# Kernel tuning notes

Hardware: AMD Instinct MI355X
Metric: run time of the kernel (lower is better)

Reference implementation:

```python
import jax, jax.numpy as jnp
import numpy as np

NUM_USERS = 200000
NUM_ITEMS = 100000
DIM = 64
NUM_LAYERS = 2
NUM_EDGES = 3200000
EPS = 1e-12  # F.normalize eps


def setup_inputs() -> dict:
    key = jax.random.key(0)
    ks = jax.random.split(key, 8)
    return {
        "user_emb": jax.random.normal(ks[0], (NUM_USERS, DIM), dtype=jnp.float32),
        "item_emb": jax.random.normal(ks[1], (NUM_ITEMS, DIM), dtype=jnp.float32),
        "Wu": jax.random.normal(ks[2], (NUM_LAYERS, DIM, 2 * DIM), dtype=jnp.float32) * 0.1,
        "Wi": jax.random.normal(ks[3], (NUM_LAYERS, DIM, 2 * DIM), dtype=jnp.float32) * 0.1,
        "u_idx": jax.random.randint(ks[4], (NUM_EDGES,), 0, NUM_USERS, dtype=jnp.int32),
        "i_idx": jax.random.randint(ks[5], (NUM_EDGES,), 0, NUM_ITEMS, dtype=jnp.int32),
        "w_u2i": jax.random.uniform(ks[6], (NUM_EDGES,), dtype=jnp.float32),
        "w_i2u": jax.random.uniform(ks[7], (NUM_EDGES,), dtype=jnp.float32),
    }


def _l2_normalize(x):
    # matches F.normalize(p=2, dim=1): x / max(||x||, eps)
    n = jnp.sqrt(jnp.sum(x * x, axis=1, keepdims=True))
    return x / jnp.maximum(n, EPS)


def _spmm(vals, rows, cols, h, num_rows):
    # (sparse [num_rows, num_cols]) @ h : gather rows of h at cols, scale, scatter-add
    msg = vals[:, None] * h[cols]  # [E, DIM]
    return jax.ops.segment_sum(msg, rows, num_segments=num_rows)


def reference(user_emb, item_emb, Wu, Wi, u_idx, i_idx, w_u2i, w_i2u):
    h_u, h_i = user_emb, item_emb
    for l in range(NUM_LAYERS):
        neigh_u = _spmm(w_u2i, u_idx, i_idx, h_i, NUM_USERS)   # adj_u2i @ h_i
        neigh_i = _spmm(w_i2u, i_idx, u_idx, h_u, NUM_ITEMS)   # adj_i2u @ h_u
        # Linear(2*dim -> dim, no bias): concat then x @ W.T
        h_u_new = jax.nn.relu(jnp.concatenate([h_u, neigh_u], axis=1) @ Wu[l].T)
        h_i_new = jax.nn.relu(jnp.concatenate([h_i, neigh_i], axis=1) @ Wi[l].T)
        h_u = _l2_normalize(h_u_new)
        h_i = _l2_normalize(h_i_new)
    return (h_u, h_i)
```

## Files before the change

kernel.cpp:

```cpp
#include <hip/hip_runtime.h>


#define N_USERS 200000
#define N_ITEMS 100000
#define N_EDGES 3200000
#define NB_U 782
#define NB_I 391

typedef float v2f __attribute__((ext_vector_type(2)));

__global__ __launch_bounds__(256) void wprep_kernel(
    const float* __restrict__ Wu, const float* __restrict__ Wi,
    float* __restrict__ WuT, float* __restrict__ WiT)
{
    int idx = blockIdx.x * 256 + threadIdx.x;
    const float* src = Wu;
    float* dst = WuT;
    int i = idx;
    if (idx >= 16384) { src = Wi; dst = WiT; i = idx - 16384; }
    int l = i >> 13;
    int r = i & 8191;
    int j = r >> 7;
    int k = r & 127;
    dst[l * 8192 + k * 64 + j] = src[i];
}

__global__ __launch_bounds__(256) void hist_kernel(
    const int* __restrict__ u_idx, const int* __restrict__ i_idx,
    int* __restrict__ deg_u, int* __restrict__ deg_i,
    unsigned short* __restrict__ rank_u, unsigned short* __restrict__ rank_i)
{
    int t = blockIdx.x * 256 + threadIdx.x;
    if (t < N_EDGES) {
        rank_u[t] = (unsigned short)atomicAdd(&deg_u[u_idx[t]], 1);
    } else {
        int e = t - N_EDGES;
        rank_i[e] = (unsigned short)atomicAdd(&deg_i[i_idx[e]], 1);
    }
}

__global__ __launch_bounds__(256) void scanA_kernel(
    const int* __restrict__ deg_u, const int* __restrict__ deg_i,
    int* __restrict__ bsum_u, int* __restrict__ bsum_i)
{
    int b = blockIdx.x;
    const int* deg; int n; int* bs; int bb;
    if (b < NB_U) { deg = deg_u; n = N_USERS; bs = bsum_u; bb = b; }
    else          { deg = deg_i; n = N_ITEMS; bs = bsum_i; bb = b - NB_U; }
    int i = bb * 256 + threadIdx.x;
    int v = (i < n) ? deg[i] : 0;
    #pragma unroll
    for (int off = 1; off < 64; off <<= 1) v += __shfl_xor(v, off);
    __shared__ int ws4[4];
    int wv = threadIdx.x >> 6;
    if ((threadIdx.x & 63) == 0) ws4[wv] = v;
    __syncthreads();
    if (threadIdx.x == 0) bs[bb] = ws4[0] + ws4[1] + ws4[2] + ws4[3];
}

__global__ __launch_bounds__(1024) void scanB_kernel(
    const int* __restrict__ bsum_u, int* __restrict__ bpre_u,
    const int* __restrict__ bsum_i, int* __restrict__ bpre_i)
{
    __shared__ int s[1024];
    const int* src; int* dst; int n;
    if (blockIdx.x == 0) { src = bsum_u; dst = bpre_u; n = NB_U; }
    else                 { src = bsum_i; dst = bpre_i; n = NB_I; }
    int t = threadIdx.x;
    int v = (t < n) ? src[t] : 0;
    s[t] = v; __syncthreads();
    #pragma unroll
    for (int off = 1; off < 1024; off <<= 1) {
        int x = (t >= off) ? s[t - off] : 0;
        __syncthreads();
        s[t] += x;
        __syncthreads();
    }
    if (t < n) dst[t] = s[t] - v;
}

__global__ __launch_bounds__(256) void scanC_kernel(
    const int* __restrict__ deg_u, const int* __restrict__ deg_i,
    const int* __restrict__ bpre_u, const int* __restrict__ bpre_i,
    int* __restrict__ rowptr_u, int* __restrict__ rowptr_i)
{
    int b = blockIdx.x;
    const int* deg; int n; const int* bpre; int* rowptr; int bb;
    if (b < NB_U) { deg = deg_u; n = N_USERS; bpre = bpre_u; rowptr = rowptr_u; bb = b; }
    else          { deg = deg_i; n = N_ITEMS; bpre = bpre_i; rowptr = rowptr_i; bb = b - NB_U; }
    int t = threadIdx.x;
    int i = bb * 256 + t;
    int d = (i < n) ? deg[i] : 0;
    __shared__ int s[256];
    s[t] = d; __syncthreads();
    #pragma unroll
    for (int off = 1; off < 256; off <<= 1) {
        int x = (t >= off) ? s[t - off] : 0;
        __syncthreads();
        s[t] += x;
        __syncthreads();
    }
    int val = bpre[bb] + (s[t] - d);
    if (i < n) rowptr[i] = val;
    if (b == 0 && t == 0) { rowptr_u[N_USERS] = N_EDGES; rowptr_i[N_ITEMS] = N_EDGES; }
}

__global__ __launch_bounds__(256) void fill_kernel(
    const int* __restrict__ u_idx, const int* __restrict__ i_idx,
    const float* __restrict__ w_u2i, const float* __restrict__ w_i2u,
    const unsigned short* __restrict__ rank_u, const unsigned short* __restrict__ rank_i,
    const int* __restrict__ rowptr_u, const int* __restrict__ rowptr_i,
    uint2* __restrict__ edges_u, uint2* __restrict__ edges_i)
{
    const int part   = blockIdx.x & 7;
    const int slot   = blockIdx.x >> 3;
    const int nslots = gridDim.x >> 3;
    const int stride = nslots * 256;

    for (int e = slot * 256 + threadIdx.x; e < N_EDGES; e += stride) {
        int ru = u_idx[e];
        int ri = i_idx[e];
        if ((ru & 7) == part) {
            int p = rowptr_u[ru] + rank_u[e];
            unsigned rl = (unsigned)(ru & 63);
            unsigned P  = (rl << 6) | (((rl >> 1) & 3) << 3);
            edges_u[p] = make_uint2((unsigned)ri | (P << 18), __float_as_uint(w_u2i[e]));
        }
        if ((ri & 7) == part) {
            int p = rowptr_i[ri] + rank_i[e];
            unsigned rl = (unsigned)(ri & 63);
            unsigned P  = (rl << 6) | (((rl >> 1) & 3) << 3);
            edges_i[p] = make_uint2((unsigned)ru | (P << 18), __float_as_uint(w_i2u[e]));
        }
    }
}

#define XSW(rr) ((((rr) >> 1) & 3) << 3)

__global__ __launch_bounds__(256) void transform_fused_kernel(
    const float* __restrict__ hself_u, const float* __restrict__ hsrc_u,
    const int* __restrict__ rowptr_u, const uint2* __restrict__ edges_u,
    const float* __restrict__ WtU, float* __restrict__ out_u,
    const float* __restrict__ hself_i, const float* __restrict__ hsrc_i,
    const int* __restrict__ rowptr_i, const uint2* __restrict__ edges_i,
    const float* __restrict__ WtI, float* __restrict__ out_i,
    int nbu)
{
    __shared__ float Ws[32 * 64];
    __shared__ float Xs[64 * 64];

    const int tid = threadIdx.x;

    const int nbt = (int)gridDim.x;
    const int nbi = nbt - nbu;
    int bid = (int)blockIdx.x;
    int g = bid / 3, r = bid - 3 * g;
    bool is_u; int bb;
    if (r < 2) {
        int cand = 2 * g + r;
        if (cand < nbu) { is_u = true;  bb = cand; }
        else            { is_u = false; bb = nbi - (nbt - bid); }
    } else {
        int cand = g;
        if (cand < nbi) { is_u = false; bb = cand; }
        else            { is_u = true;  bb = nbu - (nbt - bid); }
    }

    const float* hself; const float* hsrc; const int* rowptr;
    const uint2* edges; const float* Wt; float* out; int N;
    if (is_u) {
        hself = hself_u; hsrc = hsrc_u; rowptr = rowptr_u; edges = edges_u;
        Wt = WtU; out = out_u; N = N_USERS;
    } else {
        hself = hself_i; hsrc = hsrc_i; rowptr = rowptr_i; edges = edges_i;
        Wt = WtI; out = out_i; N = N_ITEMS;
    }
    const int row0 = bb * 64;

    const int tr = tid >> 3;
    const int tc = tid & 7;
    const int r0 = 2 * tr;
    const int xsw = XSW(r0);

    v2f acc2[2][4];
    #pragma unroll
    for (int j = 0; j < 2; ++j)
        #pragma unroll
        for (int c = 0; c < 4; ++c) acc2[j][c] = (v2f){0.f, 0.f};

    {
        const float4* wsrc = (const float4*)Wt;
        float4* wdst = (float4*)Ws;
        wdst[tid]       = wsrc[tid];
        wdst[tid + 256] = wsrc[tid + 256];
        #pragma unroll
        for (int i = 0; i < 4; ++i) {
            int idx4 = tid + i * 256;
            int rr = idx4 >> 4, c4 = idx4 & 15;
            int gr = row0 + rr; if (gr > N - 1) gr = N - 1;
            float4 v = ((const float4*)(hself + (size_t)gr * 64))[c4];
            ((float4*)Xs)[(rr << 4) + (c4 ^ (XSW(rr) >> 2))] = v;
        }
    }
    __syncthreads();

    #pragma unroll 8
    for (int k2 = 0; k2 < 32; ++k2) {
        int kk = k2;
        float a0 = Xs[(r0 << 6) + (kk ^ xsw)];
        float a1 = Xs[((r0 + 1) << 6) + (kk ^ xsw)];
        float4 b0 = *(const float4*)&Ws[k2 * 64 + 8 * tc];
        float4 b1 = *(const float4*)&Ws[k2 * 64 + 8 * tc + 4];
        v2f bv0 = {b0.x, b0.y}, bv1 = {b0.z, b0.w};
        v2f bv2 = {b1.x, b1.y}, bv3 = {b1.z, b1.w};
        v2f a0v = {a0, a0}, a1v = {a1, a1};
        acc2[0][0] += a0v * bv0; acc2[0][1] += a0v * bv1;
        acc2[0][2] += a0v * bv2; acc2[0][3] += a0v * bv3;
        acc2[1][0] += a1v * bv0; acc2[1][1] += a1v * bv1;
        acc2[1][2] += a1v * bv2; acc2[1][3] += a1v * bv3;
    }
    __syncthreads();

    {
        const float4* wsrc = (const float4*)(Wt + 2048);
        float4* wdst = (float4*)Ws;
        wdst[tid]       = wsrc[tid];
        wdst[tid + 256] = wsrc[tid + 256];
    }
    __syncthreads();

    #pragma unroll 8
    for (int k2 = 0; k2 < 32; ++k2) {
        int kk = 32 + k2;
        float a0 = Xs[(r0 << 6) + (kk ^ xsw)];
        float a1 = Xs[((r0 + 1) << 6) + (kk ^ xsw)];
        float4 b0 = *(const float4*)&Ws[k2 * 64 + 8 * tc];
        float4 b1 = *(const float4*)&Ws[k2 * 64 + 8 * tc + 4];
        v2f bv0 = {b0.x, b0.y}, bv1 = {b0.z, b0.w};
        v2f bv2 = {b1.x, b1.y}, bv3 = {b1.z, b1.w};
        v2f a0v = {a0, a0}, a1v = {a1, a1};
        acc2[0][0] += a0v * bv0; acc2[0][1] += a0v * bv1;
        acc2[0][2] += a0v * bv2; acc2[0][3] += a0v * bv3;
        acc2[1][0] += a1v * bv0; acc2[1][1] += a1v * bv1;
        acc2[1][2] += a1v * bv2; acc2[1][3] += a1v * bv3;
    }
    __syncthreads();

    {
        float4 z = make_float4(0.f, 0.f, 0.f, 0.f);
        #pragma unroll
        for (int i = 0; i < 4; ++i) ((float4*)Xs)[tid + i * 256] = z;
    }
    __syncthreads();

    {
        const int wv = tid >> 6;
        const int ln = tid & 63;
        const int e0 = rowptr[row0];
        const int e1 = rowptr[min(row0 + 64, N)];
        const int perw = (e1 - e0 + 3) >> 2;
        const int wsb  = e0 + wv * perw;
        const int web  = min(wsb + perw, e1);
        const int clen = (web - wsb + 3) >> 2;

        int cs[4], ce[4];
        uint2 ec[4];
        float gacc[4];
        unsigned curP[4];
        #pragma unroll
        for (int c = 0; c < 4; ++c) {
            cs[c] = wsb + c * clen;
            ce[c] = min(cs[c] + clen, web);
            ec[c] = edges[min(cs[c], N_EDGES - 1)];
            gacc[c] = 0.f;
        }
        #pragma unroll
        for (int c = 0; c < 4; ++c) curP[c] = (ec[c].x >> 18) & 0xFFFu;

        #pragma unroll 1
        for (int it = 0; it < clen; ++it) {
            float hv[4], w[4];
            unsigned P[4];
            #pragma unroll
            for (int c = 0; c < 4; ++c) {
                bool valid = (cs[c] + it) < ce[c];
                w[c] = valid ? __uint_as_float(ec[c].y) : 0.f;
                P[c] = (ec[c].x >> 18) & 0xFFFu;
                hv[c] = hsrc[(size_t)(ec[c].x & 0x3FFFFu) * 64 + ln];
            }
            #pragma unroll
            for (int c = 0; c < 4; ++c)
                ec[c] = edges[min(cs[c] + it + 1, N_EDGES - 1)];
            #pragma unroll
            for (int c = 0; c < 4; ++c) {
                if (P[c] != curP[c]) {
                    atomicAdd(&Xs[(int)curP[c] ^ ln], gacc[c]);
                    gacc[c] = 0.f;
                    curP[c] = P[c];
                }
                gacc[c] = fmaf(w[c], hv[c], gacc[c]);
            }
        }
        #pragma unroll
        for (int c = 0; c < 4; ++c)
            atomicAdd(&Xs[(int)curP[c] ^ ln], gacc[c]);
    }
    __syncthreads();

    {
        const float4* wsrc = (const float4*)(Wt + 4096);
        float4* wdst = (float4*)Ws;
        wdst[tid]       = wsrc[tid];
        wdst[tid + 256] = wsrc[tid + 256];
    }
    __syncthreads();

    #pragma unroll 8
    for (int k2 = 0; k2 < 32; ++k2) {
        int kk = k2;
        float a0 = Xs[(r0 << 6) + (kk ^ xsw)];
        float a1 = Xs[((r0 + 1) << 6) + (kk ^ xsw)];
        float4 b0 = *(const float4*)&Ws[k2 * 64 + 8 * tc];
        float4 b1 = *(const float4*)&Ws[k2 * 64 + 8 * tc + 4];
        v2f bv0 = {b0.x, b0.y}, bv1 = {b0.z, b0.w};
        v2f bv2 = {b1.x, b1.y}, bv3 = {b1.z, b1.w};
        v2f a0v = {a0, a0}, a1v = {a1, a1};
        acc2[0][0] += a0v * bv0; acc2[0][1] += a0v * bv1;
        acc2[0][2] += a0v * bv2; acc2[0][3] += a0v * bv3;
        acc2[1][0] += a1v * bv0; acc2[1][1] += a1v * bv1;
        acc2[1][2] += a1v * bv2; acc2[1][3] += a1v * bv3;
    }
    __syncthreads();

    {
        const float4* wsrc = (const float4*)(Wt + 6144);
        float4* wdst = (float4*)Ws;
        wdst[tid]       = wsrc[tid];
        wdst[tid + 256] = wsrc[tid + 256];
    }
    __syncthreads();

    #pragma unroll 8
    for (int k2 = 0; k2 < 32; ++k2) {
        int kk = 32 + k2;
        float a0 = Xs[(r0 << 6) + (kk ^ xsw)];
        float a1 = Xs[((r0 + 1) << 6) + (kk ^ xsw)];
        float4 b0 = *(const float4*)&Ws[k2 * 64 + 8 * tc];
        float4 b1 = *(const float4*)&Ws[k2 * 64 + 8 * tc + 4];
        v2f bv0 = {b0.x, b0.y}, bv1 = {b0.z, b0.w};
        v2f bv2 = {b1.x, b1.y}, bv3 = {b1.z, b1.w};
        v2f a0v = {a0, a0}, a1v = {a1, a1};
        acc2[0][0] += a0v * bv0; acc2[0][1] += a0v * bv1;
        acc2[0][2] += a0v * bv2; acc2[0][3] += a0v * bv3;
        acc2[1][0] += a1v * bv0; acc2[1][1] += a1v * bv1;
        acc2[1][2] += a1v * bv2; acc2[1][3] += a1v * bv3;
    }

    #pragma unroll
    for (int j = 0; j < 2; ++j) {
        float v[8];
        v[0] = fmaxf(acc2[j][0].x, 0.f); v[1] = fmaxf(acc2[j][0].y, 0.f);
        v[2] = fmaxf(acc2[j][1].x, 0.f); v[3] = fmaxf(acc2[j][1].y, 0.f);
        v[4] = fmaxf(acc2[j][2].x, 0.f); v[5] = fmaxf(acc2[j][2].y, 0.f);
        v[6] = fmaxf(acc2[j][3].x, 0.f); v[7] = fmaxf(acc2[j][3].y, 0.f);
        float s = 0.f;
        #pragma unroll
        for (int c = 0; c < 8; ++c) s = fmaf(v[c], v[c], s);
        s += __shfl_xor(s, 1);
        s += __shfl_xor(s, 2);
        s += __shfl_xor(s, 4);
        float nrm = sqrtf(s);
        float inv = 1.f / fmaxf(nrm, 1e-12f);
        int gr = row0 + r0 + j;
        if (gr < N) {
            float4 o0 = make_float4(v[0]*inv, v[1]*inv, v[2]*inv, v[3]*inv);
            float4 o1 = make_float4(v[4]*inv, v[5]*inv, v[6]*inv, v[7]*inv);
            float* p = out + gr * 64 + 8 * tc;
            *(float4*)p       = o0;
            *(float4*)(p + 4) = o1;
        }
    }
}

extern "C" void kernel_launch(void* const* d_in, const int* in_sizes, int n_in,
                              void* d_out, int out_size, void* d_ws, size_t ws_size,
                              hipStream_t stream)
{
    (void)in_sizes; (void)n_in; (void)out_size; (void)ws_size;

    const float* user_emb = (const float*)d_in[0];
    const float* item_emb = (const float*)d_in[1];
    const float* Wu       = (const float*)d_in[2];
    const float* Wi       = (const float*)d_in[3];
    const int*   u_idx    = (const int*)d_in[4];
    const int*   i_idx    = (const int*)d_in[5];
    const float* w_u2i    = (const float*)d_in[6];
    const float* w_i2u    = (const float*)d_in[7];
    float* out = (float*)d_out;

    float* ws      = (float*)d_ws;
    float* WuT     = ws;
    float* WiT     = WuT + 16384;
    float* hu1     = WiT + 16384;
    float* hi1     = hu1 + N_USERS * 64;
    uint2* edges_u = (uint2*)(hi1 + N_ITEMS * 64);
    uint2* edges_i = edges_u + N_EDGES;
    unsigned short* rank_u = (unsigned short*)(edges_i + N_EDGES);
    unsigned short* rank_i = rank_u + N_EDGES;
    int* rowptr_u = (int*)(rank_i + N_EDGES);
    int* rowptr_i = rowptr_u + (N_USERS + 1);
    int* deg_u    = rowptr_i + (N_ITEMS + 1);
    int* deg_i    = deg_u + N_USERS;
    int* bsum_u   = deg_i + N_ITEMS;
    int* bpre_u   = bsum_u + NB_U;
    int* bsum_i   = bpre_u + NB_U;
    int* bpre_i   = bsum_i + NB_I;

    const int tu_blocks = (N_USERS + 63) / 64;
    const int ti_blocks = (N_ITEMS + 63) / 64;
    const int e2_blocks = (2 * N_EDGES) / 256;

    wprep_kernel<<<128, 256, 0, stream>>>(Wu, Wi, WuT, WiT);
    hipMemsetAsync(deg_u, 0, (size_t)(N_USERS + N_ITEMS) * 4, stream);
    hist_kernel<<<e2_blocks, 256, 0, stream>>>(u_idx, i_idx, deg_u, deg_i, rank_u, rank_i);
    scanA_kernel<<<NB_U + NB_I, 256, 0, stream>>>(deg_u, deg_i, bsum_u, bsum_i);
    scanB_kernel<<<2, 1024, 0, stream>>>(bsum_u, bpre_u, bsum_i, bpre_i);
    scanC_kernel<<<NB_U + NB_I, 256, 0, stream>>>(deg_u, deg_i, bpre_u, bpre_i, rowptr_u, rowptr_i);
    fill_kernel<<<2048, 256, 0, stream>>>(u_idx, i_idx, w_u2i, w_i2u,
                                          rank_u, rank_i, rowptr_u, rowptr_i,
                                          edges_u, edges_i);

    transform_fused_kernel<<<tu_blocks + ti_blocks, 256, 0, stream>>>(
        user_emb, item_emb, rowptr_u, edges_u, WuT, hu1,
        item_emb, user_emb, rowptr_i, edges_i, WiT, hi1, tu_blocks);

    transform_fused_kernel<<<tu_blocks + ti_blocks, 256, 0, stream>>>(
        hu1, hi1, rowptr_u, edges_u, WuT + 8192, out,
        hi1, hu1, rowptr_i, edges_i, WiT + 8192, out + (size_t)N_USERS * 64, tu_blocks);
}
```

Measured before the change: 1.379 ms.

## Gather two edges per wave with float2 loads and shrink weight staging tile

The neighbor gather now has each half-wave handle a different edge, with every lane loading a float2 of two feature columns. Each wave therefore processes two edges per iteration and the loop count is halved, which increases memory-level parallelism in the gather. The weight staging buffer in shared memory is halved to 16x64, and the GEMM phases become a 4-step loop with more syncs. This lowers LDS use to allow higher occupancy, at the cost of more barriers and twice as many LDS atomics per flush.

```diff
diff --git a/kernel.cpp b/kernel.cpp
--- a/kernel.cpp
+++ b/kernel.cpp
@@ -146,7 +146,7 @@
     const float* __restrict__ WtI, float* __restrict__ out_i,
     int nbu)
 {
-    __shared__ float Ws[32 * 64];
+    __shared__ float Ws[16 * 64];
     __shared__ float Xs[64 * 64];
 
     const int tid = threadIdx.x;
@@ -189,10 +189,7 @@
         for (int c = 0; c < 4; ++c) acc2[j][c] = (v2f){0.f, 0.f};
 
     {
-        const float4* wsrc = (const float4*)Wt;
-        float4* wdst = (float4*)Ws;
-        wdst[tid]       = wsrc[tid];
-        wdst[tid + 256] = wsrc[tid + 256];
+        ((float4*)Ws)[tid] = ((const float4*)Wt)[tid];
         #pragma unroll
         for (int i = 0; i < 4; ++i) {
             int idx4 = tid + i * 256;
@@ -204,47 +201,29 @@
     }
     __syncthreads();
 
-    #pragma unroll 8
-    for (int k2 = 0; k2 < 32; ++k2) {
-        int kk = k2;
-        float a0 = Xs[(r0 << 6) + (kk ^ xsw)];
-        float a1 = Xs[((r0 + 1) << 6) + (kk ^ xsw)];
-        float4 b0 = *(const float4*)&Ws[k2 * 64 + 8 * tc];
-        float4 b1 = *(const float4*)&Ws[k2 * 64 + 8 * tc + 4];
-        v2f bv0 = {b0.x, b0.y}, bv1 = {b0.z, b0.w};
-        v2f bv2 = {b1.x, b1.y}, bv3 = {b1.z, b1.w};
-        v2f a0v = {a0, a0}, a1v = {a1, a1};
-        acc2[0][0] += a0v * bv0; acc2[0][1] += a0v * bv1;
-        acc2[0][2] += a0v * bv2; acc2[0][3] += a0v * bv3;
-        acc2[1][0] += a1v * bv0; acc2[1][1] += a1v * bv1;
-        acc2[1][2] += a1v * bv2; acc2[1][3] += a1v * bv3;
-    }
-    __syncthreads();
-
-    {
-        const float4* wsrc = (const float4*)(Wt + 2048);
-        float4* wdst = (float4*)Ws;
-        wdst[tid]       = wsrc[tid];
-        wdst[tid + 256] = wsrc[tid + 256];
-    }
-    __syncthreads();
-
-    #pragma unroll 8
-    for (int k2 = 0; k2 < 32; ++k2) {
-        int kk = 32 + k2;
-        float a0 = Xs[(r0 << 6) + (kk ^ xsw)];
-        float a1 = Xs[((r0 + 1) << 6) + (kk ^ xsw)];
-        float4 b0 = *(const float4*)&Ws[k2 * 64 + 8 * tc];
-        float4 b1 = *(const float4*)&Ws[k2 * 64 + 8 * tc + 4];
-        v2f bv0 = {b0.x, b0.y}, bv1 = {b0.z, b0.w};
-        v2f bv2 = {b1.x, b1.y}, bv3 = {b1.z, b1.w};
-        v2f a0v = {a0, a0}, a1v = {a1, a1};
-        acc2[0][0] += a0v * bv0; acc2[0][1] += a0v * bv1;
-        acc2[0][2] += a0v * bv2; acc2[0][3] += a0v * bv3;
-        acc2[1][0] += a1v * bv0; acc2[1][1] += a1v * bv1;
-        acc2[1][2] += a1v * bv2; acc2[1][3] += a1v * bv3;
-    }
-    __syncthreads();
+    #pragma unroll 1
+    for (int q = 0; q < 4; ++q) {
+        #pragma unroll
+        for (int k2 = 0; k2 < 16; ++k2) {
+            int kk = (q << 4) | k2;
+            float a0 = Xs[(r0 << 6) + (kk ^ xsw)];
+            float a1 = Xs[((r0 + 1) << 6) + (kk ^ xsw)];
+            float4 b0 = *(const float4*)&Ws[k2 * 64 + 8 * tc];
+            float4 b1 = *(const float4*)&Ws[k2 * 64 + 8 * tc + 4];
+            v2f bv0 = {b0.x, b0.y}, bv1 = {b0.z, b0.w};
+            v2f bv2 = {b1.x, b1.y}, bv3 = {b1.z, b1.w};
+            v2f a0v = {a0, a0}, a1v = {a1, a1};
+            acc2[0][0] += a0v * bv0; acc2[0][1] += a0v * bv1;
+            acc2[0][2] += a0v * bv2; acc2[0][3] += a0v * bv3;
+            acc2[1][0] += a1v * bv0; acc2[1][1] += a1v * bv1;
+            acc2[1][2] += a1v * bv2; acc2[1][3] += a1v * bv3;
+        }
+        __syncthreads();
+        if (q < 3) {
+            ((float4*)Ws)[tid] = ((const float4*)(Wt + ((q + 1) << 10)))[tid];
+            __syncthreads();
+        }
+    }
 
     {
         float4 z = make_float4(0.f, 0.f, 0.f, 0.f);
@@ -256,104 +235,91 @@
     {
         const int wv = tid >> 6;
         const int ln = tid & 63;
+        const int h  = ln >> 5;
+        const int d0 = (ln & 31) << 1;
         const int e0 = rowptr[row0];
         const int e1 = rowptr[min(row0 + 64, N)];
         const int perw = (e1 - e0 + 3) >> 2;
         const int wsb  = e0 + wv * perw;
         const int web  = min(wsb + perw, e1);
         const int clen = (web - wsb + 3) >> 2;
-
-        int cs[4], ce[4];
+        const int nit  = (clen + 1) >> 1;
+
+        int pe[4], ce[4];
         uint2 ec[4];
-        float gacc[4];
+        float2 gacc[4];
         unsigned curP[4];
         #pragma unroll
         for (int c = 0; c < 4; ++c) {
-            cs[c] = wsb + c * clen;
-            ce[c] = min(cs[c] + clen, web);
-            ec[c] = edges[min(cs[c], N_EDGES - 1)];
-            gacc[c] = 0.f;
-        }
-        #pragma unroll
-        for (int c = 0; c < 4; ++c) curP[c] = (ec[c].x >> 18) & 0xFFFu;
+            int cs = wsb + c * clen;
+            ce[c] = min(cs + clen, web);
+            pe[c] = cs + h;
+            ec[c] = edges[min(pe[c], N_EDGES - 1)];
+            gacc[c] = make_float2(0.f, 0.f);
+            curP[c] = (ec[c].x >> 18) & 0xFFFu;
+        }
 
         #pragma unroll 1
-        for (int it = 0; it < clen; ++it) {
-            float hv[4], w[4];
-            unsigned P[4];
+        for (int it = 0; it < nit; ++it) {
+            float2 hv[4]; float w[4]; unsigned P[4];
             #pragma unroll
             for (int c = 0; c < 4; ++c) {
-                bool valid = (cs[c] + it) < ce[c];
+                bool valid = pe[c] < ce[c];
                 w[c] = valid ? __uint_as_float(ec[c].y) : 0.f;
                 P[c] = (ec[c].x >> 18) & 0xFFFu;
-                hv[c] = hsrc[(size_t)(ec[c].x & 0x3FFFFu) * 64 + ln];
+                hv[c] = *(const float2*)(hsrc + (size_t)(ec[c].x & 0x3FFFFu) * 64 + d0);
             }
             #pragma unroll
             for (int c = 0; c < 4; ++c)
-                ec[c] = edges[min(cs[c] + it + 1, N_EDGES - 1)];
+                ec[c] = edges[min(pe[c] + 2, N_EDGES - 1)];
             #pragma unroll
             for (int c = 0; c < 4; ++c) {
                 if (P[c] != curP[c]) {
-                    atomicAdd(&Xs[(int)curP[c] ^ ln], gacc[c]);
-                    gacc[c] = 0.f;
+                    int wb = (int)curP[c] ^ d0;
+                    atomicAdd(&Xs[wb], gacc[c].x);
+                    atomicAdd(&Xs[wb + 1], gacc[c].y);
+                    gacc[c] = make_float2(0.f, 0.f);
                     curP[c] = P[c];
                 }
-                gacc[c] = fmaf(w[c], hv[c], gacc[c]);
+                gacc[c].x = fmaf(w[c], hv[c].x, gacc[c].x);
+                gacc[c].y = fmaf(w[c], hv[c].y, gacc[c].y);
+                pe[c] += 2;
             }
         }
         #pragma unroll
-        for (int c = 0; c < 4; ++c)
-            atomicAdd(&Xs[(int)curP[c] ^ ln], gacc[c]);
+        for (int c = 0; c < 4; ++c) {
+            int wb = (int)curP[c] ^ d0;
+            atomicAdd(&Xs[wb], gacc[c].x);
+            atomicAdd(&Xs[wb + 1], gacc[c].y);
+        }
     }
     __syncthreads();
 
-    {
-        const float4* wsrc = (const float4*)(Wt + 4096);
-        float4* wdst = (float4*)Ws;
-        wdst[tid]       = wsrc[tid];
-        wdst[tid + 256] = wsrc[tid + 256];
-    }
+    ((float4*)Ws)[tid] = ((const float4*)(Wt + 4096))[tid];
     __syncthreads();
 
-    #pragma unroll 8
-    for (int k2 = 0; k2 < 32; ++k2) {
-        int kk = k2;
-        float a0 = Xs[(r0 << 6) + (kk ^ xsw)];
-        float a1 = Xs[((r0 + 1) << 6) + (kk ^ xsw)];
-        float4 b0 = *(const float4*)&Ws[k2 * 64 + 8 * tc];
-        float4 b1 = *(const float4*)&Ws[k2 * 64 + 8 * tc + 4];
-        v2f bv0 = {b0.x, b0.y}, bv1 = {b0.z, b0.w};
-        v2f bv2 = {b1.x, b1.y}, bv3 = {b1.z, b1.w};
-        v2f a0v = {a0, a0}, a1v = {a1, a1};
-        acc2[0][0] += a0v * bv0; acc2[0][1] += a0v * bv1;
-        acc2[0][2] += a0v * bv2; acc2[0][3] += a0v * bv3;
-        acc2[1][0] += a1v * bv0; acc2[1][1] += a1v * bv1;
-        acc2[1][2] += a1v * bv2; acc2[1][3] += a1v * bv3;
-    }
-    __syncthreads();
-
-    {
-        const float4* wsrc = (const float4*)(Wt + 6144);
-        float4* wdst = (float4*)Ws;
-        wdst[tid]       = wsrc[tid];
-        wdst[tid + 256] = wsrc[tid + 256];
-    }
-    __syncthreads();
-
-    #pragma unroll 8
-    for (int k2 = 0; k2 < 32; ++k2) {
-        int kk = 32 + k2;
-        float a0 = Xs[(r0 << 6) + (kk ^ xsw)];
-        float a1 = Xs[((r0 + 1) << 6) + (kk ^ xsw)];
-        float4 b0 = *(const float4*)&Ws[k2 * 64 + 8 * tc];
-        float4 b1 = *(const float4*)&Ws[k2 * 64 + 8 * tc + 4];
-        v2f bv0 = {b0.x, b0.y}, bv1 = {b0.z, b0.w};
-        v2f bv2 = {b1.x, b1.y}, bv3 = {b1.z, b1.w};
-        v2f a0v = {a0, a0}, a1v = {a1, a1};
-        acc2[0][0] += a0v * bv0; acc2[0][1] += a0v * bv1;
-        acc2[0][2] += a0v * bv2; acc2[0][3] += a0v * bv3;
-        acc2[1][0] += a1v * bv0; acc2[1][1] += a1v * bv1;
-        acc2[1][2] += a1v * bv2; acc2[1][3] += a1v * bv3;
+    #pragma unroll 1
+    for (int q = 0; q < 4; ++q) {
+        #pragma unroll
+        for (int k2 = 0; k2 < 16; ++k2) {
+            int kk = (q << 4) | k2;
+            float a0 = Xs[(r0 << 6) + (kk ^ xsw)];
+            float a1 = Xs[((r0 + 1) << 6) + (kk ^ xsw)];
+            float4 b0 = *(const float4*)&Ws[k2 * 64 + 8 * tc];
+            float4 b1 = *(const float4*)&Ws[k2 * 64 + 8 * tc + 4];
+            v2f bv0 = {b0.x, b0.y}, bv1 = {b0.z, b0.w};
+            v2f bv2 = {b1.x, b1.y}, bv3 = {b1.z, b1.w};
+            v2f a0v = {a0, a0}, a1v = {a1, a1};
+            acc2[0][0] += a0v * bv0; acc2[0][1] += a0v * bv1;
+            acc2[0][2] += a0v * bv2; acc2[0][3] += a0v * bv3;
+            acc2[1][0] += a1v * bv0; acc2[1][1] += a1v * bv1;
+            acc2[1][2] += a1v * bv2; acc2[1][3] += a1v * bv3;
+        }
+        __syncthreads();
+        if (q < 3) {
+            ((float4*)Ws)[tid] = ((const float4*)(Wt + 4096 + ((q + 1) << 10)))[tid];
+            __syncthreads();
+        }
     }
 
     #pragma unroll
```

After: 1.472 ms. +6.8%, slower.
